# Kernel tuning notes

Measured on AMD Instinct MI355X. Metric: run time of the kernel, lower is better.

The kernel has to match this reference:

```python
import jax, jax.numpy as jnp
import numpy as np
from jax.ops import segment_sum

N_NODES = 50000
N_EDGES = 800000
HIDDEN = 96
N_CLASSES = 10
N_GRAPHS = 64


def gcn_conv(x, W, b, src, dst, num_nodes):
    """PyG GCNConv: symmetric-normalized aggregation with self-loops.
    out = D^{-1/2} (A + I) D^{-1/2} (x W) + b, with D the degree of A + I.
    Self-loop contribution handled analytically instead of appending edges.
    """
    ones = jnp.ones((src.shape[0],), dtype=x.dtype)
    deg = segment_sum(ones, dst, num_segments=num_nodes) + 1.0  # +1 for self-loop
    dinv = jax.lax.rsqrt(deg)
    h = x @ W  # [N, H] small GEMM
    norm = dinv[src] * dinv[dst]  # [E]
    msg = h[src] * norm[:, None]  # [E, H] dominant gather
    out = segment_sum(msg, dst, num_segments=num_nodes)  # scatter-add
    out = out + h * (dinv * dinv)[:, None]  # self-loop term
    return out + b


def setup_inputs() -> dict:
    key = jax.random.key(0)
    ks = jax.random.split(key, 12)
    x = jax.random.normal(ks[0], (N_NODES, HIDDEN), dtype=jnp.float32)
    edge_index = jax.random.randint(ks[1], (2, N_EDGES), 0, N_NODES, dtype=jnp.int64)
    batch = jnp.sort(jax.random.randint(ks[2], (N_NODES,), 0, N_GRAPHS, dtype=jnp.int64))
    s = 1.0 / np.sqrt(HIDDEN)
    W0 = jax.random.normal(ks[3], (HIDDEN, HIDDEN), dtype=jnp.float32) * s
    b0 = jnp.zeros((HIDDEN,), dtype=jnp.float32)
    W1 = jax.random.normal(ks[4], (HIDDEN, HIDDEN), dtype=jnp.float32) * s
    b1 = jnp.zeros((HIDDEN,), dtype=jnp.float32)
    W2 = jax.random.normal(ks[5], (HIDDEN, HIDDEN), dtype=jnp.float32) * s
    b2 = jnp.zeros((HIDDEN,), dtype=jnp.float32)
    W_lin = jax.random.normal(ks[6], (HIDDEN, N_CLASSES), dtype=jnp.float32) * s
    b_lin = jnp.zeros((N_CLASSES,), dtype=jnp.float32)
    return {"x": x, "edge_index": edge_index, "batch": batch,
            "W0": W0, "b0": b0, "W1": W1, "b1": b1, "W2": W2, "b2": b2,
            "W_lin": W_lin, "b_lin": b_lin}


def reference(x, edge_index, batch, W0, b0, W1, b1, W2, b2, W_lin, b_lin):
    src, dst = edge_index[0], edge_index[1]
    n = x.shape[0]
    h = jax.nn.relu(gcn_conv(x, W0, b0, src, dst, n))
    h = jax.nn.relu(gcn_conv(h, W1, b1, src, dst, n))
    h = gcn_conv(h, W2, b2, src, dst, n)  # last layer: no activation
    # global_mean_pool over batch index
    sums = segment_sum(h, batch, num_segments=N_GRAPHS)  # [G, H]
    cnts = segment_sum(jnp.ones((n,), dtype=h.dtype), batch, num_segments=N_GRAPHS)
    pooled = sums / jnp.maximum(cnts, 1.0)[:, None]
    # dropout is identity in eval mode
    return pooled @ W_lin + b_lin  # [G, num_classes]
```

## Files before the change

kernel.cpp:

```cpp
#include <hip/hip_runtime.h>
#include <hip/hip_bf16.h>

#define HID 96
#define NGRAPHS 64
#define SENT 0xC3C3u
#define NROWS 50116

typedef __attribute__((ext_vector_type(8))) short short8;
typedef __attribute__((ext_vector_type(4))) float floatx4;
typedef __attribute__((ext_vector_type(8))) unsigned short ushort8v;

__device__ __forceinline__ float bf16_to_f32(unsigned short u) {
    unsigned int v = ((unsigned int)u) << 16;
    return __builtin_bit_cast(float, v);
}
__device__ __forceinline__ unsigned short f32_to_bf16(float f) {
    unsigned int u = __builtin_bit_cast(unsigned int, f);
    u += 0x7fff + ((u >> 16) & 1);
    return (unsigned short)(u >> 16);
}

__device__ __forceinline__ void gather_batch(const unsigned short* __restrict__ h,
                                             const unsigned short* __restrict__ csr,
                                             int i, int fi, float& a0, float& a1) {
    ushort8v iv = *(const ushort8v*)(csr + i);
    ushort2 v0 = *(const ushort2*)(h + (size_t)iv[0] * HID + fi);
    ushort2 v1 = *(const ushort2*)(h + (size_t)iv[1] * HID + fi);
    ushort2 v2 = *(const ushort2*)(h + (size_t)iv[2] * HID + fi);
    ushort2 v3 = *(const ushort2*)(h + (size_t)iv[3] * HID + fi);
    ushort2 v4 = *(const ushort2*)(h + (size_t)iv[4] * HID + fi);
    ushort2 v5 = *(const ushort2*)(h + (size_t)iv[5] * HID + fi);
    ushort2 v6 = *(const ushort2*)(h + (size_t)iv[6] * HID + fi);
    ushort2 v7 = *(const ushort2*)(h + (size_t)iv[7] * HID + fi);
    a0 += bf16_to_f32(v0.x) + bf16_to_f32(v1.x) + bf16_to_f32(v2.x) +
          bf16_to_f32(v3.x) + bf16_to_f32(v4.x) + bf16_to_f32(v5.x) +
          bf16_to_f32(v6.x) + bf16_to_f32(v7.x);
    a1 += bf16_to_f32(v0.y) + bf16_to_f32(v1.y) + bf16_to_f32(v2.y) +
          bf16_to_f32(v3.y) + bf16_to_f32(v4.y) + bf16_to_f32(v5.y) +
          bf16_to_f32(v6.y) + bf16_to_f32(v7.y);
}

__device__ __forceinline__ void gather2(const unsigned short* __restrict__ h,
                                        const unsigned short* __restrict__ csr,
                                        int i0, int e0, int i1, int e1, int fi,
                                        float& a00, float& a01, float& a10,
                                        float& a11) {
    while (i0 < e0 && i1 < e1) {
        ushort8v ca = *(const ushort8v*)(csr + i0);
        ushort8v cb = *(const ushort8v*)(csr + i1);
        i0 += 8;
        i1 += 8;
        ushort2 u0 = *(const ushort2*)(h + (size_t)ca[0] * HID + fi);
        ushort2 u1 = *(const ushort2*)(h + (size_t)ca[1] * HID + fi);
        ushort2 u2 = *(const ushort2*)(h + (size_t)ca[2] * HID + fi);
        ushort2 u3 = *(const ushort2*)(h + (size_t)ca[3] * HID + fi);
        ushort2 u4 = *(const ushort2*)(h + (size_t)ca[4] * HID + fi);
        ushort2 u5 = *(const ushort2*)(h + (size_t)ca[5] * HID + fi);
        ushort2 u6 = *(const ushort2*)(h + (size_t)ca[6] * HID + fi);
        ushort2 u7 = *(const ushort2*)(h + (size_t)ca[7] * HID + fi);
        ushort2 w0 = *(const ushort2*)(h + (size_t)cb[0] * HID + fi);
        ushort2 w1 = *(const ushort2*)(h + (size_t)cb[1] * HID + fi);
        ushort2 w2 = *(const ushort2*)(h + (size_t)cb[2] * HID + fi);
        ushort2 w3 = *(const ushort2*)(h + (size_t)cb[3] * HID + fi);
        ushort2 w4 = *(const ushort2*)(h + (size_t)cb[4] * HID + fi);
        ushort2 w5 = *(const ushort2*)(h + (size_t)cb[5] * HID + fi);
        ushort2 w6 = *(const ushort2*)(h + (size_t)cb[6] * HID + fi);
        ushort2 w7 = *(const ushort2*)(h + (size_t)cb[7] * HID + fi);
        a00 += bf16_to_f32(u0.x) + bf16_to_f32(u1.x) + bf16_to_f32(u2.x) +
               bf16_to_f32(u3.x) + bf16_to_f32(u4.x) + bf16_to_f32(u5.x) +
               bf16_to_f32(u6.x) + bf16_to_f32(u7.x);
        a01 += bf16_to_f32(u0.y) + bf16_to_f32(u1.y) + bf16_to_f32(u2.y) +
               bf16_to_f32(u3.y) + bf16_to_f32(u4.y) + bf16_to_f32(u5.y) +
               bf16_to_f32(u6.y) + bf16_to_f32(u7.y);
        a10 += bf16_to_f32(w0.x) + bf16_to_f32(w1.x) + bf16_to_f32(w2.x) +
               bf16_to_f32(w3.x) + bf16_to_f32(w4.x) + bf16_to_f32(w5.x) +
               bf16_to_f32(w6.x) + bf16_to_f32(w7.x);
        a11 += bf16_to_f32(w0.y) + bf16_to_f32(w1.y) + bf16_to_f32(w2.y) +
               bf16_to_f32(w3.y) + bf16_to_f32(w4.y) + bf16_to_f32(w5.y) +
               bf16_to_f32(w6.y) + bf16_to_f32(w7.y);
    }
    for (; i0 < e0; i0 += 8) gather_batch(h, csr, i0, fi, a00, a01);
    for (; i1 < e1; i1 += 8) gather_batch(h, csr, i1, fi, a10, a11);
}

__global__ __launch_bounds__(256) void init_kernel(
    int* __restrict__ deg, float* __restrict__ psum,
    unsigned short* __restrict__ bufA, unsigned short* __restrict__ bufB, int N) {
    int i = blockIdx.x * 256 + threadIdx.x;
    if (i < N) deg[i] = 0;
    if (i < NGRAPHS * HID + NGRAPHS) psum[i] = 0.0f;
    if (i < HID) {
        bufA[(size_t)SENT * HID + i] = 0;
        bufB[(size_t)SENT * HID + i] = 0;
    }
}

__global__ void deg_kernel(const int* __restrict__ dst, int* __restrict__ deg,
                           int n_edges) {
    int t = blockIdx.x * blockDim.x + threadIdx.x;
    int e0 = t * 4;
    if (e0 + 4 <= n_edges) {
        int4 d4 = *(const int4*)(dst + e0);
        atomicAdd(&deg[d4.x], 1);
        atomicAdd(&deg[d4.y], 1);
        atomicAdd(&deg[d4.z], 1);
        atomicAdd(&deg[d4.w], 1);
    } else {
        for (int e = e0; e < n_edges; e++) atomicAdd(&deg[dst[e]], 1);
    }
}

__global__ __launch_bounds__(256) void scan_phaseA(const int* __restrict__ deg,
                                                   float* __restrict__ dinv,
                                                   int* __restrict__ blocksum,
                                                   int N) {
    int i = blockIdx.x * 256 + threadIdx.x;
    int d = (i < N) ? deg[i] : 0;
    if (i < N) dinv[i] = rsqrtf((float)d + 1.0f);
    int v = (d + 7) & ~7;
#pragma unroll
    for (int off = 32; off > 0; off >>= 1) v += __shfl_down(v, off, 64);
    __shared__ int s[4];
    if ((threadIdx.x & 63) == 0) s[threadIdx.x >> 6] = v;
    __syncthreads();
    if (threadIdx.x == 0) blocksum[blockIdx.x] = s[0] + s[1] + s[2] + s[3];
}

__global__ __launch_bounds__(256) void scan_phaseC(const int* __restrict__ deg,
                                                   const int* __restrict__ blocksum,
                                                   int* __restrict__ rowptr,
                                                   int* __restrict__ cursor,
                                                   int N, int NB) {
    int t = threadIdx.x;
    int mine = (t < NB && t < blockIdx.x) ? blocksum[t] : 0;
#pragma unroll
    for (int off = 32; off > 0; off >>= 1) mine += __shfl_down(mine, off, 64);
    __shared__ int ps[4];
    if ((t & 63) == 0) ps[t >> 6] = mine;
    __syncthreads();
    int pref = ps[0] + ps[1] + ps[2] + ps[3];

    __shared__ int s[256];
    int i = blockIdx.x * 256 + t;
    int own = (i < N) ? (deg[i] + 7) & ~7 : 0;
    s[t] = own;
    __syncthreads();
#pragma unroll
    for (int off = 1; off < 256; off <<= 1) {
        int v = (t >= off) ? s[t - off] : 0;
        __syncthreads();
        s[t] += v;
        __syncthreads();
    }
    if (i < N) {
        int r = pref + s[t] - own;
        rowptr[i] = r;
        cursor[i] = r;
        if (i == N - 1) rowptr[N] = r + own;
    }
}

__global__ void csr_fill(const int* __restrict__ src, const int* __restrict__ dst,
                         int* __restrict__ cursor,
                         unsigned short* __restrict__ csr_src, int n_edges) {
    int t = blockIdx.x * blockDim.x + threadIdx.x;
    int e0 = t * 8;
    if (e0 + 8 <= n_edges) {
        int4 da = *(const int4*)(dst + e0);
        int4 db = *(const int4*)(dst + e0 + 4);
        int4 sa = *(const int4*)(src + e0);
        int4 sb = *(const int4*)(src + e0 + 4);
        int p0 = atomicAdd(&cursor[da.x], 1);
        int p1 = atomicAdd(&cursor[da.y], 1);
        int p2 = atomicAdd(&cursor[da.z], 1);
        int p3 = atomicAdd(&cursor[da.w], 1);
        int p4 = atomicAdd(&cursor[db.x], 1);
        int p5 = atomicAdd(&cursor[db.y], 1);
        int p6 = atomicAdd(&cursor[db.z], 1);
        int p7 = atomicAdd(&cursor[db.w], 1);
        csr_src[p0] = (unsigned short)sa.x;
        csr_src[p1] = (unsigned short)sa.y;
        csr_src[p2] = (unsigned short)sa.z;
        csr_src[p3] = (unsigned short)sa.w;
        csr_src[p4] = (unsigned short)sb.x;
        csr_src[p5] = (unsigned short)sb.y;
        csr_src[p6] = (unsigned short)sb.z;
        csr_src[p7] = (unsigned short)sb.w;
    } else {
        for (int e = e0; e < n_edges; e++) {
            int p = atomicAdd(&cursor[dst[e]], 1);
            csr_src[p] = (unsigned short)src[e];
        }
    }
}

__global__ void swizzle_W(const float* __restrict__ W0, const float* __restrict__ W1,
                          const float* __restrict__ W2, unsigned short* __restrict__ Wz) {
    const float* W = (blockIdx.x == 0) ? W0 : (blockIdx.x == 1) ? W1 : W2;
    unsigned short* dst = Wz + blockIdx.x * HID * HID;
    for (int e = threadIdx.x; e < HID * HID; e += blockDim.x) {
        int k = e / HID, n = e % HID;
        int nt = n >> 4, kki = k >> 5, quad = (k >> 3) & 3, j = k & 7;
        int lane = (n & 15) | (quad << 4);
        dst[(((nt * 3 + kki) * 64 + lane) << 3) | j] = f32_to_bf16(W[e]);
    }
}

__global__ __launch_bounds__(256) void gemm0_f32(
    const float* __restrict__ X, const unsigned short* __restrict__ Wz,
    const float* __restrict__ dinv, unsigned short* __restrict__ Out, int Mtiles) {
    int wv = threadIdx.x >> 6;
    int lane = threadIdx.x & 63;
    int quad = lane >> 4;
    int mrow = lane & 15;
    int tt = blockIdx.x * 2 + (wv >> 1);
    int half = wv & 1;
    if (tt >= Mtiles) return;

    short8 bfrag[9];
    const short8* Wz8 = (const short8*)Wz;
#pragma unroll
    for (int f = 0; f < 9; f++) bfrag[f] = Wz8[(half * 9 + f) * 64 + lane];

    int m0 = tt * 16;
    const float* arow = X + (size_t)(m0 + mrow) * HID + quad * 8;
    short8 a[3];
#pragma unroll
    for (int kb = 0; kb < 3; kb++) {
        float4 u = *(const float4*)(arow + kb * 32);
        float4 v = *(const float4*)(arow + kb * 32 + 4);
        short8 t;
        t[0] = (short)f32_to_bf16(u.x); t[1] = (short)f32_to_bf16(u.y);
        t[2] = (short)f32_to_bf16(u.z); t[3] = (short)f32_to_bf16(u.w);
        t[4] = (short)f32_to_bf16(v.x); t[5] = (short)f32_to_bf16(v.y);
        t[6] = (short)f32_to_bf16(v.z); t[7] = (short)f32_to_bf16(v.w);
        a[kb] = t;
    }
    float dscale[4];
#pragma unroll
    for (int r = 0; r < 4; r++) dscale[r] = dinv[m0 + quad * 4 + r];
    unsigned short* orow = Out + (size_t)m0 * HID;
#pragma unroll
    for (int ntl = 0; ntl < 3; ntl++) {
        int nt = half * 3 + ntl;
        floatx4 c = {0.0f, 0.0f, 0.0f, 0.0f};
        c = __builtin_amdgcn_mfma_f32_16x16x32_bf16(a[0], bfrag[ntl * 3 + 0], c, 0, 0, 0);
        c = __builtin_amdgcn_mfma_f32_16x16x32_bf16(a[1], bfrag[ntl * 3 + 1], c, 0, 0, 0);
        c = __builtin_amdgcn_mfma_f32_16x16x32_bf16(a[2], bfrag[ntl * 3 + 2], c, 0, 0, 0);
#pragma unroll
        for (int r = 0; r < 4; r++)
            orow[(size_t)(quad * 4 + r) * HID + nt * 16 + mrow] =
                f32_to_bf16(c[r] * dscale[r]);
    }
}

__global__ __launch_bounds__(256) void fused_gather_gemm(
    const unsigned short* __restrict__ h, const int* __restrict__ rowptr,
    const unsigned short* __restrict__ csr, const float* __restrict__ dinv,
    const float* __restrict__ bias, const unsigned short* __restrict__ Wz,
    unsigned short* __restrict__ Out, int Mtiles) {
    __shared__ unsigned short tile[2][16][104];
    int wv = threadIdx.x >> 6;
    int lane = threadIdx.x & 63;
    int quad = lane >> 4;
    int mrow = lane & 15;
    int tsel = wv >> 1;
    int half = wv & 1;
    int tt = blockIdx.x * 2 + tsel;
    bool active = tt < Mtiles;
    int fi = (lane < 48) ? lane * 2 : 94;

    if (active) {
        float b0 = bias[fi], b1 = bias[fi + 1];
        int n0 = tt * 16;
        for (int jj = 0; jj < 8; jj += 2) {
            int j0 = half * 8 + jj;
            int na = n0 + j0;
            int nb = na + 1;
            int ia = rowptr[na];
            int ea = rowptr[na + 1];
            int ib = ea;
            int eb = rowptr[nb + 1];
            float da = dinv[na], db = dinv[nb];
            ushort2 ha = *(const ushort2*)(h + (size_t)na * HID + fi);
            ushort2 hb = *(const ushort2*)(h + (size_t)nb * HID + fi);
            float a00 = bf16_to_f32(ha.x), a01 = bf16_to_f32(ha.y);
            float a10 = bf16_to_f32(hb.x), a11 = bf16_to_f32(hb.y);
            gather2(h, csr, ia, ea, ib, eb, fi, a00, a01, a10, a11);
            a00 = fmaxf(a00 * da + b0, 0.0f);
            a01 = fmaxf(a01 * da + b1, 0.0f);
            a10 = fmaxf(a10 * db + b0, 0.0f);
            a11 = fmaxf(a11 * db + b1, 0.0f);
            if (lane < 48) {
                tile[tsel][j0][fi] = f32_to_bf16(a00);
                tile[tsel][j0][fi + 1] = f32_to_bf16(a01);
                tile[tsel][j0 + 1][fi] = f32_to_bf16(a10);
                tile[tsel][j0 + 1][fi + 1] = f32_to_bf16(a11);
            }
        }
    }
    __syncthreads();
    if (!active) return;

    short8 bfrag[9];
    const short8* Wz8 = (const short8*)Wz;
#pragma unroll
    for (int f = 0; f < 9; f++) bfrag[f] = Wz8[(half * 9 + f) * 64 + lane];

    const unsigned short* tp = &tile[tsel][0][0];
    short8 a[3];
#pragma unroll
    for (int kb = 0; kb < 3; kb++)
        a[kb] = *(const short8*)(tp + mrow * 104 + quad * 8 + kb * 32);
    int n0 = tt * 16;
    float dscale[4];
#pragma unroll
    for (int r = 0; r < 4; r++) dscale[r] = dinv[n0 + quad * 4 + r];
    unsigned short* orow = Out + (size_t)n0 * HID;
#pragma unroll
    for (int ntl = 0; ntl < 3; ntl++) {
        int nt = half * 3 + ntl;
        floatx4 c = {0.0f, 0.0f, 0.0f, 0.0f};
        c = __builtin_amdgcn_mfma_f32_16x16x32_bf16(a[0], bfrag[ntl * 3 + 0], c, 0, 0, 0);
        c = __builtin_amdgcn_mfma_f32_16x16x32_bf16(a[1], bfrag[ntl * 3 + 1], c, 0, 0, 0);
        c = __builtin_amdgcn_mfma_f32_16x16x32_bf16(a[2], bfrag[ntl * 3 + 2], c, 0, 0, 0);
#pragma unroll
        for (int r = 0; r < 4; r++)
            orow[(size_t)(quad * 4 + r) * HID + nt * 16 + mrow] =
                f32_to_bf16(c[r] * dscale[r]);
    }
}

__global__ __launch_bounds__(256) void gather_pool(
    const unsigned short* __restrict__ h, const int* __restrict__ rowptr,
    const unsigned short* __restrict__ csr, const float* __restrict__ dinv,
    const float* __restrict__ bias, const int* __restrict__ batch,
    float* __restrict__ psum, float* __restrict__ pcnt, int Ntiles8) {
    int wv = threadIdx.x >> 6;
    int lane = threadIdx.x & 63;
    int tt = blockIdx.x * 4 + wv;
    if (tt >= Ntiles8) return;
    int fi = (lane < 48) ? lane * 2 : 94;
    float b0 = bias[fi], b1 = bias[fi + 1];

    int n0 = tt * 8;
    int g_cur = batch[n0];
    float s0 = 0.0f, s1 = 0.0f;
    int cnt = 0;
    for (int jj = 0; jj < 8; jj += 2) {
        int na = n0 + jj;
        int nb = na + 1;
        int ia = rowptr[na];
        int ea = rowptr[na + 1];
        int ib = ea;
        int eb = rowptr[nb + 1];
        float da = dinv[na], db = dinv[nb];
        ushort2 ha = *(const ushort2*)(h + (size_t)na * HID + fi);
        ushort2 hb = *(const ushort2*)(h + (size_t)nb * HID + fi);
        float a00 = bf16_to_f32(ha.x), a01 = bf16_to_f32(ha.y);
        float a10 = bf16_to_f32(hb.x), a11 = bf16_to_f32(hb.y);
        gather2(h, csr, ia, ea, ib, eb, fi, a00, a01, a10, a11);
        a00 = a00 * da + b0;
        a01 = a01 * da + b1;
        a10 = a10 * db + b0;
        a11 = a11 * db + b1;
        int ga = batch[na];
        if (ga != g_cur) {
            if (lane < 48) {
                atomicAdd(&psum[g_cur * HID + fi], s0);
                atomicAdd(&psum[g_cur * HID + fi + 1], s1);
            }
            if (lane == 0) atomicAdd(&pcnt[g_cur], (float)cnt);
            s0 = 0.0f; s1 = 0.0f; cnt = 0;
            g_cur = ga;
        }
        s0 += a00; s1 += a01; cnt++;
        int gb = batch[nb];
        if (gb != g_cur) {
            if (lane < 48) {
                atomicAdd(&psum[g_cur * HID + fi], s0);
                atomicAdd(&psum[g_cur * HID + fi + 1], s1);
            }
            if (lane == 0) atomicAdd(&pcnt[g_cur], (float)cnt);
            s0 = 0.0f; s1 = 0.0f; cnt = 0;
            g_cur = gb;
        }
        s0 += a10; s1 += a11; cnt++;
    }
    if (lane < 48) {
        atomicAdd(&psum[g_cur * HID + fi], s0);
        atomicAdd(&psum[g_cur * HID + fi + 1], s1);
    }
    if (lane == 0) atomicAdd(&pcnt[g_cur], (float)cnt);
}

__global__ __launch_bounds__(640) void final_kernel(
    const float* __restrict__ sums, const float* __restrict__ cnts,
    const float* __restrict__ Wlin, const float* __restrict__ blin,
    float* __restrict__ out) {
    int t = threadIdx.x;
    if (t >= NGRAPHS * 10) return;
    int g = t / 10;
    int c = t % 10;
    float denom = fmaxf(cnts[g], 1.0f);
    float acc = blin[c];
#pragma unroll
    for (int f = 0; f < HID; f++)
        acc += (sums[g * HID + f] / denom) * Wlin[f * 10 + c];
    out[t] = acc;
}

extern "C" void kernel_launch(void* const* d_in, const int* in_sizes, int n_in,
                              void* d_out, int out_size, void* d_ws,
                              size_t ws_size, hipStream_t stream) {
    const float* x = (const float*)d_in[0];
    const int* edge = (const int*)d_in[1];
    const int* batch = (const int*)d_in[2];
    const float* W[3] = {(const float*)d_in[3], (const float*)d_in[5],
                         (const float*)d_in[7]};
    const float* B[3] = {(const float*)d_in[4], (const float*)d_in[6],
                         (const float*)d_in[8]};
    const float* Wlin = (const float*)d_in[9];
    const float* blin = (const float*)d_in[10];
    float* out = (float*)d_out;

    int N = in_sizes[0] / HID;
    int E = in_sizes[1] / 2;
    const int* src = edge;
    const int* dst = edge + E;
    int NB = (N + 255) / 256;

    char* ws = (char*)d_ws;
    size_t off = 0;
    auto alloc = [&](size_t bytes) {
        void* p = ws + off;
        off += (bytes + 255) & ~(size_t)255;
        return p;
    };
    int* deg = (int*)alloc((size_t)N * 4);
    float* dinv = (float*)alloc((size_t)N * 4);
    int* rowptr = (int*)alloc(((size_t)N + 1) * 4);
    int* cursor = (int*)alloc((size_t)N * 4);
    int* blocksum = (int*)alloc((size_t)NB * 4);
    size_t csr_cap = (size_t)E + 8 * (size_t)N;
    unsigned short* csr_src = (unsigned short*)alloc(csr_cap * 2 + 64);
    unsigned short* Wz = (unsigned short*)alloc(3 * HID * HID * 2);
    unsigned short* bufA = (unsigned short*)alloc((size_t)NROWS * HID * 2);
    unsigned short* bufB = (unsigned short*)alloc((size_t)NROWS * HID * 2);
    float* psum = (float*)alloc((NGRAPHS * HID + NGRAPHS) * 4);
    float* pcnt = psum + NGRAPHS * HID;

    hipMemsetAsync(csr_src, 0xC3, csr_cap * 2, stream);
    init_kernel<<<NB, 256, 0, stream>>>(deg, psum, bufA, bufB, N);
    deg_kernel<<<(E / 4 + 255) / 256, 256, 0, stream>>>(dst, deg, E);
    scan_phaseA<<<NB, 256, 0, stream>>>(deg, dinv, blocksum, N);
    scan_phaseC<<<NB, 256, 0, stream>>>(deg, blocksum, rowptr, cursor, N, NB);
    csr_fill<<<(E / 8 + 255) / 256, 256, 0, stream>>>(src, dst, cursor, csr_src, E);
    swizzle_W<<<3, 256, 0, stream>>>(W[0], W[1], W[2], Wz);

    int Mtiles = (N + 15) / 16;
    int grid2 = (Mtiles + 1) / 2;
    int Ntiles8 = (N + 7) / 8;
    int gridp = (Ntiles8 + 3) / 4;

    gemm0_f32<<<grid2, 256, 0, stream>>>(x, Wz, dinv, bufA, Mtiles);
    fused_gather_gemm<<<grid2, 256, 0, stream>>>(
        bufA, rowptr, csr_src, dinv, B[0], Wz + 1 * HID * HID, bufB, Mtiles);
    fused_gather_gemm<<<grid2, 256, 0, stream>>>(
        bufB, rowptr, csr_src, dinv, B[1], Wz + 2 * HID * HID, bufA, Mtiles);
    gather_pool<<<gridp, 256, 0, stream>>>(bufA, rowptr, csr_src, dinv, B[2],
                                           batch, psum, pcnt, Ntiles8);
    final_kernel<<<1, 640, 0, stream>>>(psum, pcnt, Wlin, blin, out);
}
```

Baseline: 309.3 us.

## Gather 16-byte feature chunks with 16-lane groups per node pair

Replaces the per-wave node-pair gather (each lane loading 2 bf16 features per neighbor) with a layout where each 16-lane group handles a node pair and each lane loads 8 bf16 features per neighbor row as one 16-byte load. Neighbor index prefetching is software-pipelined, and the two adjacent nodes' contiguous CSR ranges are processed as one range with predicated accumulation. The iteration count is the maximum over the wave. The pooling kernel stages results in shared memory before the segmented reduction. This aims to raise memory-level parallelism and load width in the dominant gather, at the cost of divergent trip counts and wasted lanes (12 of 16 active).

```diff
diff --git a/kernel.cpp b/kernel.cpp
--- a/kernel.cpp
+++ b/kernel.cpp
@@ -20,67 +20,51 @@
     return (unsigned short)(u >> 16);
 }
 
-__device__ __forceinline__ void gather_batch(const unsigned short* __restrict__ h,
-                                             const unsigned short* __restrict__ csr,
-                                             int i, int fi, float& a0, float& a1) {
-    ushort8v iv = *(const ushort8v*)(csr + i);
-    ushort2 v0 = *(const ushort2*)(h + (size_t)iv[0] * HID + fi);
-    ushort2 v1 = *(const ushort2*)(h + (size_t)iv[1] * HID + fi);
-    ushort2 v2 = *(const ushort2*)(h + (size_t)iv[2] * HID + fi);
-    ushort2 v3 = *(const ushort2*)(h + (size_t)iv[3] * HID + fi);
-    ushort2 v4 = *(const ushort2*)(h + (size_t)iv[4] * HID + fi);
-    ushort2 v5 = *(const ushort2*)(h + (size_t)iv[5] * HID + fi);
-    ushort2 v6 = *(const ushort2*)(h + (size_t)iv[6] * HID + fi);
-    ushort2 v7 = *(const ushort2*)(h + (size_t)iv[7] * HID + fi);
-    a0 += bf16_to_f32(v0.x) + bf16_to_f32(v1.x) + bf16_to_f32(v2.x) +
-          bf16_to_f32(v3.x) + bf16_to_f32(v4.x) + bf16_to_f32(v5.x) +
-          bf16_to_f32(v6.x) + bf16_to_f32(v7.x);
-    a1 += bf16_to_f32(v0.y) + bf16_to_f32(v1.y) + bf16_to_f32(v2.y) +
-          bf16_to_f32(v3.y) + bf16_to_f32(v4.y) + bf16_to_f32(v5.y) +
-          bf16_to_f32(v6.y) + bf16_to_f32(v7.y);
-}
-
-__device__ __forceinline__ void gather2(const unsigned short* __restrict__ h,
-                                        const unsigned short* __restrict__ csr,
-                                        int i0, int e0, int i1, int e1, int fi,
-                                        float& a00, float& a01, float& a10,
-                                        float& a11) {
-    while (i0 < e0 && i1 < e1) {
-        ushort8v ca = *(const ushort8v*)(csr + i0);
-        ushort8v cb = *(const ushort8v*)(csr + i1);
-        i0 += 8;
-        i1 += 8;
-        ushort2 u0 = *(const ushort2*)(h + (size_t)ca[0] * HID + fi);
-        ushort2 u1 = *(const ushort2*)(h + (size_t)ca[1] * HID + fi);
-        ushort2 u2 = *(const ushort2*)(h + (size_t)ca[2] * HID + fi);
-        ushort2 u3 = *(const ushort2*)(h + (size_t)ca[3] * HID + fi);
-        ushort2 u4 = *(const ushort2*)(h + (size_t)ca[4] * HID + fi);
-        ushort2 u5 = *(const ushort2*)(h + (size_t)ca[5] * HID + fi);
-        ushort2 u6 = *(const ushort2*)(h + (size_t)ca[6] * HID + fi);
-        ushort2 u7 = *(const ushort2*)(h + (size_t)ca[7] * HID + fi);
-        ushort2 w0 = *(const ushort2*)(h + (size_t)cb[0] * HID + fi);
-        ushort2 w1 = *(const ushort2*)(h + (size_t)cb[1] * HID + fi);
-        ushort2 w2 = *(const ushort2*)(h + (size_t)cb[2] * HID + fi);
-        ushort2 w3 = *(const ushort2*)(h + (size_t)cb[3] * HID + fi);
-        ushort2 w4 = *(const ushort2*)(h + (size_t)cb[4] * HID + fi);
-        ushort2 w5 = *(const ushort2*)(h + (size_t)cb[5] * HID + fi);
-        ushort2 w6 = *(const ushort2*)(h + (size_t)cb[6] * HID + fi);
-        ushort2 w7 = *(const ushort2*)(h + (size_t)cb[7] * HID + fi);
-        a00 += bf16_to_f32(u0.x) + bf16_to_f32(u1.x) + bf16_to_f32(u2.x) +
-               bf16_to_f32(u3.x) + bf16_to_f32(u4.x) + bf16_to_f32(u5.x) +
-               bf16_to_f32(u6.x) + bf16_to_f32(u7.x);
-        a01 += bf16_to_f32(u0.y) + bf16_to_f32(u1.y) + bf16_to_f32(u2.y) +
-               bf16_to_f32(u3.y) + bf16_to_f32(u4.y) + bf16_to_f32(u5.y) +
-               bf16_to_f32(u6.y) + bf16_to_f32(u7.y);
-        a10 += bf16_to_f32(w0.x) + bf16_to_f32(w1.x) + bf16_to_f32(w2.x) +
-               bf16_to_f32(w3.x) + bf16_to_f32(w4.x) + bf16_to_f32(w5.x) +
-               bf16_to_f32(w6.x) + bf16_to_f32(w7.x);
-        a11 += bf16_to_f32(w0.y) + bf16_to_f32(w1.y) + bf16_to_f32(w2.y) +
-               bf16_to_f32(w3.y) + bf16_to_f32(w4.y) + bf16_to_f32(w5.y) +
-               bf16_to_f32(w6.y) + bf16_to_f32(w7.y);
-    }
-    for (; i0 < e0; i0 += 8) gather_batch(h, csr, i0, fi, a00, a01);
-    for (; i1 < e1; i1 += 8) gather_batch(h, csr, i1, fi, a10, a11);
+__device__ __forceinline__ void gather_core(
+    const unsigned short* __restrict__ h, const unsigned short* __restrict__ csr,
+    int r0, int r1, int r2, int TAIL, int it2, int pe8,
+    float* __restrict__ aA, float* __restrict__ aB) {
+    int s = r0;
+    ushort8v i0 = *(const ushort8v*)(csr + (s < r2 ? s : TAIL));
+    ushort8v i1 = *(const ushort8v*)(csr + (s + 8 < r2 ? s + 8 : TAIL));
+    for (int it = 0; it < it2; ++it) {
+        ushort8v v0[8], v1[8];
+#pragma unroll
+        for (int j = 0; j < 8; ++j)
+            v0[j] = *(const ushort8v*)(h + (int)i0[j] * HID + pe8);
+#pragma unroll
+        for (int j = 0; j < 8; ++j)
+            v1[j] = *(const ushort8v*)(h + (int)i1[j] * HID + pe8);
+        int sn = s + 16;
+        ushort8v n0 = *(const ushort8v*)(csr + (sn < r2 ? sn : TAIL));
+        ushort8v n1 = *(const ushort8v*)(csr + (sn + 8 < r2 ? sn + 8 : TAIL));
+        bool cA0 = s < r1;
+        bool cA1 = (s + 8) < r1;
+        float t0[8], t1[8];
+#pragma unroll
+        for (int f = 0; f < 8; ++f) {
+            t0[f] = bf16_to_f32(v0[0][f]) + bf16_to_f32(v0[1][f]) +
+                    bf16_to_f32(v0[2][f]) + bf16_to_f32(v0[3][f]) +
+                    bf16_to_f32(v0[4][f]) + bf16_to_f32(v0[5][f]) +
+                    bf16_to_f32(v0[6][f]) + bf16_to_f32(v0[7][f]);
+            t1[f] = bf16_to_f32(v1[0][f]) + bf16_to_f32(v1[1][f]) +
+                    bf16_to_f32(v1[2][f]) + bf16_to_f32(v1[3][f]) +
+                    bf16_to_f32(v1[4][f]) + bf16_to_f32(v1[5][f]) +
+                    bf16_to_f32(v1[6][f]) + bf16_to_f32(v1[7][f]);
+        }
+#pragma unroll
+        for (int f = 0; f < 8; ++f) {
+            float x0 = cA0 ? t0[f] : 0.0f;
+            aA[f] += x0;
+            aB[f] += t0[f] - x0;
+            float x1 = cA1 ? t1[f] : 0.0f;
+            aA[f] += x1;
+            aB[f] += t1[f] - x1;
+        }
+        i0 = n0;
+        i1 = n1;
+        s = sn;
+    }
 }
 
 __global__ __launch_bounds__(256) void init_kernel(
@@ -258,7 +242,7 @@
     const unsigned short* __restrict__ h, const int* __restrict__ rowptr,
     const unsigned short* __restrict__ csr, const float* __restrict__ dinv,
     const float* __restrict__ bias, const unsigned short* __restrict__ Wz,
-    unsigned short* __restrict__ Out, int Mtiles) {
+    unsigned short* __restrict__ Out, int Mtiles, int N) {
     __shared__ unsigned short tile[2][16][104];
     int wv = threadIdx.x >> 6;
     int lane = threadIdx.x & 63;
@@ -268,35 +252,43 @@
     int half = wv & 1;
     int tt = blockIdx.x * 2 + tsel;
     bool active = tt < Mtiles;
-    int fi = (lane < 48) ? lane * 2 : 94;
+    int g = lane >> 4;
+    int p = lane & 15;
+    int pe = (p < 12) ? p : 11;
+    int pe8 = pe * 8;
 
     if (active) {
-        float b0 = bias[fi], b1 = bias[fi + 1];
-        int n0 = tt * 16;
-        for (int jj = 0; jj < 8; jj += 2) {
-            int j0 = half * 8 + jj;
-            int na = n0 + j0;
-            int nb = na + 1;
-            int ia = rowptr[na];
-            int ea = rowptr[na + 1];
-            int ib = ea;
-            int eb = rowptr[nb + 1];
-            float da = dinv[na], db = dinv[nb];
-            ushort2 ha = *(const ushort2*)(h + (size_t)na * HID + fi);
-            ushort2 hb = *(const ushort2*)(h + (size_t)nb * HID + fi);
-            float a00 = bf16_to_f32(ha.x), a01 = bf16_to_f32(ha.y);
-            float a10 = bf16_to_f32(hb.x), a11 = bf16_to_f32(hb.y);
-            gather2(h, csr, ia, ea, ib, eb, fi, a00, a01, a10, a11);
-            a00 = fmaxf(a00 * da + b0, 0.0f);
-            a01 = fmaxf(a01 * da + b1, 0.0f);
-            a10 = fmaxf(a10 * db + b0, 0.0f);
-            a11 = fmaxf(a11 * db + b1, 0.0f);
-            if (lane < 48) {
-                tile[tsel][j0][fi] = f32_to_bf16(a00);
-                tile[tsel][j0][fi + 1] = f32_to_bf16(a01);
-                tile[tsel][j0 + 1][fi] = f32_to_bf16(a10);
-                tile[tsel][j0 + 1][fi + 1] = f32_to_bf16(a11);
+        int TAIL = rowptr[N];
+        int j0 = half * 8 + g * 2;
+        int na = tt * 16 + j0;
+        int r0 = rowptr[na], r1 = rowptr[na + 1], r2 = rowptr[na + 2];
+        float da = dinv[na], db = dinv[na + 1];
+        float aA[8], aB[8];
+        ushort8v sva = *(const ushort8v*)(h + (size_t)na * HID + pe8);
+        ushort8v svb = *(const ushort8v*)(h + (size_t)(na + 1) * HID + pe8);
+#pragma unroll
+        for (int f = 0; f < 8; ++f) {
+            aA[f] = bf16_to_f32(sva[f]);
+            aB[f] = bf16_to_f32(svb[f]);
+        }
+        int it2 = (r2 - r0 + 15) >> 4;
+        int o = __shfl_xor(it2, 16, 64);
+        it2 = it2 > o ? it2 : o;
+        o = __shfl_xor(it2, 32, 64);
+        it2 = it2 > o ? it2 : o;
+        gather_core(h, csr, r0, r1, r2, TAIL, it2, pe8, aA, aB);
+        float4 bb0 = *(const float4*)(bias + pe8);
+        float4 bb1 = *(const float4*)(bias + pe8 + 4);
+        float bv[8] = {bb0.x, bb0.y, bb0.z, bb0.w, bb1.x, bb1.y, bb1.z, bb1.w};
+        if (p < 12) {
+            ushort8v oA, oB;
+#pragma unroll
+            for (int f = 0; f < 8; ++f) {
+                oA[f] = f32_to_bf16(fmaxf(aA[f] * da + bv[f], 0.0f));
+                oB[f] = f32_to_bf16(fmaxf(aB[f] * db + bv[f], 0.0f));
             }
+            *(ushort8v*)(&tile[tsel][j0][pe8]) = oA;
+            *(ushort8v*)(&tile[tsel][j0 + 1][pe8]) = oB;
         }
     }
     __syncthreads();
@@ -335,47 +327,62 @@
     const unsigned short* __restrict__ h, const int* __restrict__ rowptr,
     const unsigned short* __restrict__ csr, const float* __restrict__ dinv,
     const float* __restrict__ bias, const int* __restrict__ batch,
-    float* __restrict__ psum, float* __restrict__ pcnt, int Ntiles8) {
+    float* __restrict__ psum, float* __restrict__ pcnt, int Ntiles8, int N) {
+    __shared__ float stage[4][8][96];
     int wv = threadIdx.x >> 6;
     int lane = threadIdx.x & 63;
     int tt = blockIdx.x * 4 + wv;
     if (tt >= Ntiles8) return;
+    int g = lane >> 4;
+    int p = lane & 15;
+    int pe = (p < 12) ? p : 11;
+    int pe8 = pe * 8;
+
+    int TAIL = rowptr[N];
+    int n0 = tt * 8;
+    int na = n0 + g * 2;
+    int r0 = rowptr[na], r1 = rowptr[na + 1], r2 = rowptr[na + 2];
+    float da = dinv[na], db = dinv[na + 1];
+    float aA[8], aB[8];
+    ushort8v sva = *(const ushort8v*)(h + (size_t)na * HID + pe8);
+    ushort8v svb = *(const ushort8v*)(h + (size_t)(na + 1) * HID + pe8);
+#pragma unroll
+    for (int f = 0; f < 8; ++f) {
+        aA[f] = bf16_to_f32(sva[f]);
+        aB[f] = bf16_to_f32(svb[f]);
+    }
+    int it2 = (r2 - r0 + 15) >> 4;
+    int o = __shfl_xor(it2, 16, 64);
+    it2 = it2 > o ? it2 : o;
+    o = __shfl_xor(it2, 32, 64);
+    it2 = it2 > o ? it2 : o;
+    gather_core(h, csr, r0, r1, r2, TAIL, it2, pe8, aA, aB);
+    float4 bb0 = *(const float4*)(bias + pe8);
+    float4 bb1 = *(const float4*)(bias + pe8 + 4);
+    float bv[8] = {bb0.x, bb0.y, bb0.z, bb0.w, bb1.x, bb1.y, bb1.z, bb1.w};
+    if (p < 12) {
+        floatx4 oa0 = {aA[0] * da + bv[0], aA[1] * da + bv[1],
+                       aA[2] * da + bv[2], aA[3] * da + bv[3]};
+        floatx4 oa1 = {aA[4] * da + bv[4], aA[5] * da + bv[5],
+                       aA[6] * da + bv[6], aA[7] * da + bv[7]};
+        floatx4 ob0 = {aB[0] * db + bv[0], aB[1] * db + bv[1],
+                       aB[2] * db + bv[2], aB[3] * db + bv[3]};
+        floatx4 ob1 = {aB[4] * db + bv[4], aB[5] * db + bv[5],
+                       aB[6] * db + bv[6], aB[7] * db + bv[7]};
+        *(floatx4*)(&stage[wv][g * 2][pe8]) = oa0;
+        *(floatx4*)(&stage[wv][g * 2][pe8 + 4]) = oa1;
+        *(floatx4*)(&stage[wv][g * 2 + 1][pe8]) = ob0;
+        *(floatx4*)(&stage[wv][g * 2 + 1][pe8 + 4]) = ob1;
+    }
+    asm volatile("s_waitcnt lgkmcnt(0)" ::: "memory");
+
     int fi = (lane < 48) ? lane * 2 : 94;
-    float b0 = bias[fi], b1 = bias[fi + 1];
-
-    int n0 = tt * 8;
     int g_cur = batch[n0];
     float s0 = 0.0f, s1 = 0.0f;
     int cnt = 0;
-    for (int jj = 0; jj < 8; jj += 2) {
-        int na = n0 + jj;
-        int nb = na + 1;
-        int ia = rowptr[na];
-        int ea = rowptr[na + 1];
-        int ib = ea;
-        int eb = rowptr[nb + 1];
-        float da = dinv[na], db = dinv[nb];
-        ushort2 ha = *(const ushort2*)(h + (size_t)na * HID + fi);
-        ushort2 hb = *(const ushort2*)(h + (size_t)nb * HID + fi);
-        float a00 = bf16_to_f32(ha.x), a01 = bf16_to_f32(ha.y);
-        float a10 = bf16_to_f32(hb.x), a11 = bf16_to_f32(hb.y);
-        gather2(h, csr, ia, ea, ib, eb, fi, a00, a01, a10, a11);
-        a00 = a00 * da + b0;
-        a01 = a01 * da + b1;
-        a10 = a10 * db + b0;
-        a11 = a11 * db + b1;
-        int ga = batch[na];
-        if (ga != g_cur) {
-            if (lane < 48) {
-                atomicAdd(&psum[g_cur * HID + fi], s0);
-                atomicAdd(&psum[g_cur * HID + fi + 1], s1);
-            }
-            if (lane == 0) atomicAdd(&pcnt[g_cur], (float)cnt);
-            s0 = 0.0f; s1 = 0.0f; cnt = 0;
-            g_cur = ga;
-        }
-        s0 += a00; s1 += a01; cnt++;
-        int gb = batch[nb];
+#pragma unroll
+    for (int j = 0; j < 8; ++j) {
+        int gb = batch[n0 + j];
         if (gb != g_cur) {
             if (lane < 48) {
                 atomicAdd(&psum[g_cur * HID + fi], s0);
@@ -385,7 +392,9 @@
             s0 = 0.0f; s1 = 0.0f; cnt = 0;
             g_cur = gb;
         }
-        s0 += a10; s1 += a11; cnt++;
+        s0 += stage[wv][j][fi];
+        s1 += stage[wv][j][fi + 1];
+        cnt++;
     }
     if (lane < 48) {
         atomicAdd(&psum[g_cur * HID + fi], s0);
@@ -465,10 +474,10 @@
 
     gemm0_f32<<<grid2, 256, 0, stream>>>(x, Wz, dinv, bufA, Mtiles);
     fused_gather_gemm<<<grid2, 256, 0, stream>>>(
-        bufA, rowptr, csr_src, dinv, B[0], Wz + 1 * HID * HID, bufB, Mtiles);
+        bufA, rowptr, csr_src, dinv, B[0], Wz + 1 * HID * HID, bufB, Mtiles, N);
     fused_gather_gemm<<<grid2, 256, 0, stream>>>(
-        bufB, rowptr, csr_src, dinv, B[1], Wz + 2 * HID * HID, bufA, Mtiles);
+        bufB, rowptr, csr_src, dinv, B[1], Wz + 2 * HID * HID, bufA, Mtiles, N);
     gather_pool<<<gridp, 256, 0, stream>>>(bufA, rowptr, csr_src, dinv, B[2],
-                                           batch, psum, pcnt, Ntiles8);
+                                           batch, psum, pcnt, Ntiles8, N);
     final_kernel<<<1, 640, 0, stream>>>(psum, pcnt, Wlin, blin, out);
 }
```

Measured after the change: 310.0 us. Within noise of the previous version (+0.2%).
